# Kernel tuning notes

Measured on AMD Instinct MI355X. Metric: run time of the kernel, lower is better.

The kernel has to match this reference:

```python
import jax, jax.numpy as jnp
import numpy as np

B, T, E, H = 4, 2048, 1024, 16
S = E // H

def setup_inputs() -> dict:
    key = jax.random.key(0)
    ks = jax.random.split(key, 4)
    x = jax.random.normal(ks[0], (B, T, E), dtype=jnp.float32)
    Wk = jax.random.normal(ks[1], (E, E), dtype=jnp.float32) * (E ** -0.5)
    Wq = jax.random.normal(ks[2], (E, E), dtype=jnp.float32) * (E ** -0.5)
    Wo = jax.random.normal(ks[3], (E, E), dtype=jnp.float32) * (E ** -0.5)
    bo = jnp.zeros((E,), dtype=jnp.float32)
    return {"x": x, "Wk": Wk, "Wq": Wq, "Wo": Wo, "bo": bo}

def reference(x, Wk, Wq, Wo, bo):
    b, t, e = x.shape
    h, s = H, E // H
    scale = e ** (-0.25)  # original scales q and k each by e**(1/4)
    k = (x @ Wk).reshape(b, t, h, s).transpose(0, 2, 1, 3)  # bhts
    q = (x @ Wq).reshape(b, t, h, s).transpose(0, 2, 1, 3)
    # FAITHFUL to source: values use the KEYS projection (bug in original)
    v = (x @ Wk).reshape(b, t, h, s).transpose(0, 2, 1, 3)
    dot = jnp.einsum('bhqd,bhkd->bhqk', q * scale, k * scale)
    attn = jax.nn.softmax(dot, axis=-1)
    out = jnp.einsum('bhqk,bhkd->bhqd', attn, v)
    out = out.transpose(0, 2, 1, 3).reshape(b, t, e)
    return out @ Wo + bo
```

## Files before the change

kernel.cpp:

```cpp
#include <hip/hip_runtime.h>
#include <hip/hip_bf16.h>
#include <stdint.h>

static constexpr int kB = 4;
static constexpr int kT = 2048;
static constexpr int kE = 1024;
static constexpr int kH = 16;
static constexpr int kS = 64;
static constexpr int kRows = kB * kT;

typedef __attribute__((ext_vector_type(4)))  float    f32x4;
typedef __attribute__((ext_vector_type(16))) float    f32x16;
typedef __attribute__((ext_vector_type(4)))  float    float4v;
typedef __attribute__((ext_vector_type(8)))  __bf16   bf16x8;
typedef __attribute__((ext_vector_type(8)))  short    short8v;
typedef __attribute__((ext_vector_type(4)))  short    short4v;
typedef __attribute__((ext_vector_type(2)))  unsigned u32x2;

typedef const __attribute__((address_space(1))) void gvoid_t;
typedef __attribute__((address_space(3))) void lvoid_t;

__device__ __forceinline__ short f2bf(float f) {
  union { float f; unsigned u; } c; c.f = f;
  unsigned r = (c.u + 0x7FFFu + ((c.u >> 16) & 1u)) >> 16;
  return (short)(r & 0xFFFFu);
}

__device__ __forceinline__ short bfc(float f) {
  union { __bf16 b; short s; } u; u.b = (__bf16)f; return u.s;
}

__device__ __forceinline__ unsigned cvt_pk(float lo, float hi) {
  unsigned r;
  asm("v_cvt_pk_bf16_f32 %0, %1, %2" : "=v"(r) : "v"(lo), "v"(hi));
  return r;
}

__device__ __forceinline__ void plane_swap(unsigned& a, unsigned& b) {
  asm("v_permlane32_swap_b32 %0, %1" : "+v"(a), "+v"(b));
}

#if __has_builtin(__builtin_amdgcn_exp2f)
__device__ __forceinline__ float fexp2(float x) { return __builtin_amdgcn_exp2f(x); }
#else
__device__ __forceinline__ float fexp2(float x) { return exp2f(x); }
#endif

__global__ void cvt_bf16(const float* __restrict__ in, short* __restrict__ out) {
  size_t i = (size_t)(blockIdx.x * blockDim.x + threadIdx.x) * 4;
  float4v x = *(const float4v*)(in + i);
  short4v o;
  o[0] = f2bf(x[0]); o[1] = f2bf(x[1]); o[2] = f2bf(x[2]); o[3] = f2bf(x[3]);
  *(short4v*)(out + i) = o;
}

__global__ void transpose_cvt(const float* __restrict__ W, short* __restrict__ WT) {
  __shared__ float tile[32][33];
  const int tx = threadIdx.x & 31, ty = threadIdx.x >> 5;
  const int c = blockIdx.x * 32, r = blockIdx.y * 32;
  #pragma unroll
  for (int i = ty; i < 32; i += 8)
    tile[i][tx] = W[(size_t)(r + i) * kE + c + tx];
  __syncthreads();
  #pragma unroll
  for (int i = ty; i < 32; i += 8)
    WT[(size_t)(c + i) * kE + r + tx] = f2bf(tile[tx][i]);
}

__global__ __launch_bounds__(256)
void transv(const short* __restrict__ Kb, short* __restrict__ KT) {
  __shared__ short tile[64][72];
  const int tid = threadIdx.x;
  const int bh = blockIdx.y;
  const int t0 = blockIdx.x * 64;
  const size_t base = (size_t)(bh >> 4) * kT * kE + (size_t)(bh & 15) * kS;
  #pragma unroll
  for (int i = 0; i < 2; ++i) {
    const int row = i * 32 + (tid >> 3), c = (tid & 7) * 8;
    *(short8v*)&tile[row][c] =
        *(const short8v*)(Kb + base + (size_t)(t0 + row) * kE + c);
  }
  __syncthreads();
  #pragma unroll
  for (int i = 0; i < 2; ++i) {
    const int s = i * 32 + (tid >> 3), c = (tid & 7) * 8;
    short8v o;
    #pragma unroll
    for (int j = 0; j < 8; ++j) o[j] = tile[c + j][s];
    *(short8v*)(KT + ((size_t)bh * 64 + s) * kT + t0 + c) = o;
  }
}

__global__ __launch_bounds__(256)
void gemm_kq(const short* __restrict__ A, const short* __restrict__ BT,
             short* __restrict__ Kb, short* __restrict__ Qb, float qs) {
  __shared__ short As[128 * 64];
  __shared__ short Bs[128 * 64];
  const int tid = threadIdx.x;
  const int w = tid >> 6, lane = tid & 63;
  const int g = lane >> 4, lr = lane & 15;
  const int bid = blockIdx.x;
  const int id = (bid & 7) * 128 + (bid >> 3);
  const int n0 = (id & 15) * 128, m0 = (id >> 4) * 128;
  const int wr = w >> 1, wc = w & 1;
  const int srow = lane >> 3, sch = lane & 7;
  const int swz = lr & 7;

  f32x4 acc[4][4];
  #pragma unroll
  for (int m = 0; m < 4; ++m)
    #pragma unroll
    for (int n = 0; n < 4; ++n)
      #pragma unroll
      for (int r = 0; r < 4; ++r) acc[m][n][r] = 0.f;

  for (int kt = 0; kt < kE; kt += 64) {
    #pragma unroll
    for (int i = 0; i < 4; ++i) {
      const int slot = w * 4 + i;
      const int row = slot * 8 + srow;
      const int sc = sch ^ srow;
      __builtin_amdgcn_global_load_lds(
          (gvoid_t*)(A + (size_t)(m0 + row) * kE + kt + 8 * sc),
          (lvoid_t*)(As + slot * 512), 16, 0, 0);
      __builtin_amdgcn_global_load_lds(
          (gvoid_t*)(BT + (size_t)(n0 + row) * kE + kt + 8 * sc),
          (lvoid_t*)(Bs + slot * 512), 16, 0, 0);
    }
    __syncthreads();
    #pragma unroll
    for (int kk = 0; kk < 2; ++kk) {
      bf16x8 af[4], bfr[4];
      #pragma unroll
      for (int m = 0; m < 4; ++m)
        af[m] = *(const bf16x8*)(As + (wr * 64 + m * 16 + lr) * 64 + (((4 * kk + g) ^ swz) << 3));
      #pragma unroll
      for (int n = 0; n < 4; ++n)
        bfr[n] = *(const bf16x8*)(Bs + (wc * 64 + n * 16 + lr) * 64 + (((4 * kk + g) ^ swz) << 3));
      __builtin_amdgcn_s_setprio(1);
      #pragma unroll
      for (int m = 0; m < 4; ++m)
        #pragma unroll
        for (int n = 0; n < 4; ++n)
          acc[m][n] = __builtin_amdgcn_mfma_f32_16x16x32_bf16(af[m], bfr[n], acc[m][n], 0, 0, 0);
      __builtin_amdgcn_s_setprio(0);
    }
    __syncthreads();
  }

  short* C = (n0 < 1024) ? Kb : Qb;
  const float scale = (n0 < 1024) ? 1.0f : qs;
  const int crow = m0 + wr * 64, ccol = (n0 & 1023) + wc * 64;
  #pragma unroll
  for (int m = 0; m < 4; ++m)
    #pragma unroll
    for (int n = 0; n < 4; ++n)
      #pragma unroll
      for (int r = 0; r < 4; ++r)
        C[(size_t)(crow + m * 16 + 4 * g + r) * kE + ccol + n * 16 + lr] =
            bfc(acc[m][n][r] * scale);
}

__global__ __launch_bounds__(256)
void gemm_bt(const short* __restrict__ A, const short* __restrict__ BT,
             float* __restrict__ C, const float* __restrict__ bias,
             int M, int N, int K) {
  __shared__ short As[128 * 64];
  __shared__ short Bs[128 * 64];
  const int tid = threadIdx.x;
  const int w = tid >> 6, lane = tid & 63;
  const int g = lane >> 4, lr = lane & 15;
  const int bid = blockIdx.x;
  const int id = (bid & 7) * 64 + (bid >> 3);
  const int n0 = (id & 7) * 128, m0 = (id >> 3) * 128;
  const int wr = w >> 1, wc = w & 1;
  const int srow = lane >> 3, sch = lane & 7;
  const int swz = lr & 7;

  f32x4 acc[4][4];
  #pragma unroll
  for (int m = 0; m < 4; ++m)
    #pragma unroll
    for (int n = 0; n < 4; ++n)
      #pragma unroll
      for (int r = 0; r < 4; ++r) acc[m][n][r] = 0.f;

  for (int kt = 0; kt < K; kt += 64) {
    #pragma unroll
    for (int i = 0; i < 4; ++i) {
      const int slot = w * 4 + i;
      const int row = slot * 8 + srow;
      const int sc = sch ^ srow;
      __builtin_amdgcn_global_load_lds(
          (gvoid_t*)(A + (size_t)(m0 + row) * K + kt + 8 * sc),
          (lvoid_t*)(As + slot * 512), 16, 0, 0);
      __builtin_amdgcn_global_load_lds(
          (gvoid_t*)(BT + (size_t)(n0 + row) * K + kt + 8 * sc),
          (lvoid_t*)(Bs + slot * 512), 16, 0, 0);
    }
    __syncthreads();
    #pragma unroll
    for (int kk = 0; kk < 2; ++kk) {
      bf16x8 af[4], bfr[4];
      #pragma unroll
      for (int m = 0; m < 4; ++m)
        af[m] = *(const bf16x8*)(As + (wr * 64 + m * 16 + lr) * 64 + (((4 * kk + g) ^ swz) << 3));
      #pragma unroll
      for (int n = 0; n < 4; ++n)
        bfr[n] = *(const bf16x8*)(Bs + (wc * 64 + n * 16 + lr) * 64 + (((4 * kk + g) ^ swz) << 3));
      __builtin_amdgcn_s_setprio(1);
      #pragma unroll
      for (int m = 0; m < 4; ++m)
        #pragma unroll
        for (int n = 0; n < 4; ++n)
          acc[m][n] = __builtin_amdgcn_mfma_f32_16x16x32_bf16(af[m], bfr[n], acc[m][n], 0, 0, 0);
      __builtin_amdgcn_s_setprio(0);
    }
    __syncthreads();
  }

  const int crow = m0 + wr * 64, ccol = n0 + wc * 64;
  float bv[4];
  #pragma unroll
  for (int n = 0; n < 4; ++n) bv[n] = bias[ccol + n * 16 + lr];
  #pragma unroll
  for (int m = 0; m < 4; ++m)
    #pragma unroll
    for (int n = 0; n < 4; ++n)
      #pragma unroll
      for (int r = 0; r < 4; ++r)
        C[(size_t)(crow + m * 16 + 4 * g + r) * N + ccol + n * 16 + lr] =
            acc[m][n][r] + bv[n];
}

__global__ __launch_bounds__(256, 4)
void attn_kernel(const short* Qb, const short* __restrict__ Kb,
                 const short* __restrict__ KT, short* AO) {
  __shared__ short SM[16384];

  const int tid = threadIdx.x;
  const int w = tid >> 6, lane = tid & 63;
  const int l31 = lane & 31, hi = lane >> 5;
  const int swz = l31 & 7;
  const int bid = blockIdx.x;
  const int id = (bid & 7) * 128 + (bid >> 3);
  const int q0 = (id & 15) * 128;
  const int bh = id >> 4;
  const size_t base = (size_t)(bh >> 4) * kT * kE + (size_t)(bh & 15) * kS;
  const short* Kbh = Kb + base;
  const short* KTbh = KT + (size_t)bh * 64 * kT;

  const int srow_lo = lane >> 3, sch = lane & 7;

  #pragma unroll
  for (int i = 0; i < 2; ++i) {
    const int slot = w * 2 + i, row = slot * 8 + srow_lo;
    const int sc = sch ^ (row & 7);
    __builtin_amdgcn_global_load_lds(
        (gvoid_t*)(Kbh + (size_t)row * kE + 8 * sc),
        (lvoid_t*)(SM + slot * 512), 16, 0, 0);
    __builtin_amdgcn_global_load_lds(
        (gvoid_t*)(KTbh + (size_t)row * kT + 8 * sc),
        (lvoid_t*)(SM + 8192 + slot * 512), 16, 0, 0);
  }

  bf16x8 qB[4];
  #pragma unroll
  for (int ks = 0; ks < 4; ++ks)
    qB[ks] = *(const bf16x8*)(Qb + base +
        (size_t)(q0 + w * 32 + l31) * kE + ks * 16 + hi * 8);

  f32x16 oacc[2];
  #pragma unroll
  for (int r = 0; r < 16; ++r) { oacc[0][r] = 0.f; oacc[1][r] = 0.f; }
  float lsum = 0.f;

  for (int t = 0; t < 32; ++t) {
    __syncthreads();

    if (t < 31) {
      const short* kbt = Kbh + (size_t)(t + 1) * 64 * kE;
      const short* vtt = KTbh + (size_t)(t + 1) * 64;
      short* KtN = SM + ((t + 1) & 1) * 4096;
      short* VtN = SM + 8192 + ((t + 1) & 1) * 4096;
      #pragma unroll
      for (int i = 0; i < 2; ++i) {
        const int slot = w * 2 + i, row = slot * 8 + srow_lo;
        const int sc = sch ^ (row & 7);
        __builtin_amdgcn_global_load_lds(
            (gvoid_t*)(kbt + (size_t)row * kE + 8 * sc),
            (lvoid_t*)(KtN + slot * 512), 16, 0, 0);
        __builtin_amdgcn_global_load_lds(
            (gvoid_t*)(vtt + (size_t)row * kT + 8 * sc),
            (lvoid_t*)(VtN + slot * 512), 16, 0, 0);
      }
    }

    const short* KtC = SM + (t & 1) * 4096;
    const short* VtC = SM + 8192 + (t & 1) * 4096;

    f32x16 sacc[2];
    #pragma unroll
    for (int r = 0; r < 16; ++r) { sacc[0][r] = 0.f; sacc[1][r] = 0.f; }
    #pragma unroll
    for (int ks = 0; ks < 4; ++ks) {
      const int pc = ((2 * ks + hi) ^ swz) << 3;
      bf16x8 kf0 = *(const bf16x8*)(KtC + (l31)      * 64 + pc);
      bf16x8 kf1 = *(const bf16x8*)(KtC + (32 + l31) * 64 + pc);
      __builtin_amdgcn_s_setprio(1);
      sacc[0] = __builtin_amdgcn_mfma_f32_32x32x16_bf16(kf0, qB[ks], sacc[0], 0, 0, 0);
      sacc[1] = __builtin_amdgcn_mfma_f32_32x32x16_bf16(kf1, qB[ks], sacc[1], 0, 0, 0);
      __builtin_amdgcn_s_setprio(0);
    }

    union { unsigned u[4]; bf16x8 v; } pf[4];
    #pragma unroll
    for (int kvf = 0; kvf < 2; ++kvf) {
      float pe[16];
      #pragma unroll
      for (int r = 0; r < 16; ++r) {
        pe[r] = fexp2(sacc[kvf][r]);
        lsum += pe[r];
      }
      #pragma unroll
      for (int sub = 0; sub < 2; ++sub) {
        unsigned a0 = cvt_pk(pe[8 * sub + 0], pe[8 * sub + 1]);
        unsigned b0 = cvt_pk(pe[8 * sub + 4], pe[8 * sub + 5]);
        plane_swap(a0, b0);
        unsigned a1 = cvt_pk(pe[8 * sub + 2], pe[8 * sub + 3]);
        unsigned b1 = cvt_pk(pe[8 * sub + 6], pe[8 * sub + 7]);
        plane_swap(a1, b1);
        pf[2 * kvf + sub].u[0] = a0;
        pf[2 * kvf + sub].u[1] = a1;
        pf[2 * kvf + sub].u[2] = b0;
        pf[2 * kvf + sub].u[3] = b1;
      }
    }

    #pragma unroll
    for (int ks = 0; ks < 4; ++ks) {
      const int pc = ((2 * ks + hi) ^ swz) << 3;
      bf16x8 vf0 = *(const bf16x8*)(VtC + (l31)      * 64 + pc);
      bf16x8 vf1 = *(const bf16x8*)(VtC + (32 + l31) * 64 + pc);
      __builtin_amdgcn_s_setprio(1);
      oacc[0] = __builtin_amdgcn_mfma_f32_32x32x16_bf16(vf0, pf[ks].v, oacc[0], 0, 0, 0);
      oacc[1] = __builtin_amdgcn_mfma_f32_32x32x16_bf16(vf1, pf[ks].v, oacc[1], 0, 0, 0);
      __builtin_amdgcn_s_setprio(0);
    }
  }

  __syncthreads();

  const float ltot = lsum + __shfl_xor(lsum, 32);
  const float inv = 1.f / ltot;
  short* OtW = SM + w * 2176;
  #pragma unroll
  for (int sf = 0; sf < 2; ++sf)
    #pragma unroll
    for (int c = 0; c < 4; ++c) {
      u32x2 e;
      e[0] = cvt_pk(oacc[sf][4 * c + 0] * inv, oacc[sf][4 * c + 1] * inv);
      e[1] = cvt_pk(oacc[sf][4 * c + 2] * inv, oacc[sf][4 * c + 3] * inv);
      *(u32x2*)(OtW + l31 * 68 + sf * 32 + 8 * c + 4 * hi) = e;
    }
  __builtin_amdgcn_s_barrier();
  #pragma unroll
  for (int i = 0; i < 8; ++i) {
    const int row = i * 4 + (lane >> 4);
    u32x2 v = *(const u32x2*)(OtW + row * 68 + (lane & 15) * 4);
    *(u32x2*)(AO + base + (size_t)(q0 + w * 32 + row) * kE + (lane & 15) * 4) = v;
  }
}

extern "C" void kernel_launch(void* const* d_in, const int* in_sizes, int n_in,
                              void* d_out, int out_size, void* d_ws, size_t ws_size,
                              hipStream_t stream) {
  const float* x  = (const float*)d_in[0];
  const float* Wk = (const float*)d_in[1];
  const float* Wq = (const float*)d_in[2];
  const float* Wo = (const float*)d_in[3];
  const float* bo = (const float*)d_in[4];
  float* out = (float*)d_out;

  const size_t nXE = (size_t)kRows * kE;
  const size_t nW  = (size_t)kE * kE;

  short* Xb   = (short*)d_ws;
  short* Kb   = Xb   + nXE;
  short* Qb   = Kb   + nXE;
  short* WkqT = Qb   + nXE;
  short* WoT  = WkqT + 2 * nW;
  short* KTb  = Xb;
  short* AO   = Qb;

  cvt_bf16<<<dim3(nXE / (4 * 256)), 256, 0, stream>>>(x, Xb);
  transpose_cvt<<<dim3(32, 32), 256, 0, stream>>>(Wk, WkqT);
  transpose_cvt<<<dim3(32, 32), 256, 0, stream>>>(Wq, WkqT + nW);
  transpose_cvt<<<dim3(32, 32), 256, 0, stream>>>(Wo, WoT);

  gemm_kq<<<dim3(1024), 256, 0, stream>>>(
      Xb, WkqT, Kb, Qb, 0.03125f * 1.44269504f);

  transv<<<dim3(kT / 64, kB * kH), 256, 0, stream>>>(Kb, KTb);

  attn_kernel<<<dim3(1024), 256, 0, stream>>>(Qb, Kb, KTb, AO);

  gemm_bt<<<dim3(512), 256, 0, stream>>>(
      AO, WoT, out, bo, kRows, kE, kE);
}
```

Before: 177.4 us.

## Fuse prep conversions into one kernel and emit transposed K from GEMM epilogue

```diff
diff --git a/kernel.cpp b/kernel.cpp
--- a/kernel.cpp
+++ b/kernel.cpp
@@ -16,6 +16,7 @@
 typedef __attribute__((ext_vector_type(8)))  short    short8v;
 typedef __attribute__((ext_vector_type(4)))  short    short4v;
 typedef __attribute__((ext_vector_type(2)))  unsigned u32x2;
+typedef __attribute__((ext_vector_type(4)))  unsigned u32x4;
 
 typedef const __attribute__((address_space(1))) void gvoid_t;
 typedef __attribute__((address_space(3))) void lvoid_t;
@@ -46,18 +47,27 @@
 __device__ __forceinline__ float fexp2(float x) { return exp2f(x); }
 #endif
 
-__global__ void cvt_bf16(const float* __restrict__ in, short* __restrict__ out) {
-  size_t i = (size_t)(blockIdx.x * blockDim.x + threadIdx.x) * 4;
-  float4v x = *(const float4v*)(in + i);
-  short4v o;
-  o[0] = f2bf(x[0]); o[1] = f2bf(x[1]); o[2] = f2bf(x[2]); o[3] = f2bf(x[3]);
-  *(short4v*)(out + i) = o;
-}
-
-__global__ void transpose_cvt(const float* __restrict__ W, short* __restrict__ WT) {
+__global__ __launch_bounds__(256)
+void prep(const float* __restrict__ x, const float* __restrict__ Wk,
+          const float* __restrict__ Wq, const float* __restrict__ Wo,
+          short* __restrict__ Xb, short* __restrict__ WkqT,
+          short* __restrict__ WoT) {
+  const int bid = blockIdx.x;
+  if (bid < 8192) {
+    size_t i = ((size_t)bid * 256 + threadIdx.x) * 4;
+    float4v v = *(const float4v*)(x + i);
+    short4v o;
+    o[0] = f2bf(v[0]); o[1] = f2bf(v[1]); o[2] = f2bf(v[2]); o[3] = f2bf(v[3]);
+    *(short4v*)(Xb + i) = o;
+    return;
+  }
   __shared__ float tile[32][33];
+  const int tb = bid - 8192;
+  const int which = tb >> 10, t = tb & 1023;
+  const float* W = (which == 0) ? Wk : ((which == 1) ? Wq : Wo);
+  short* WT = (which == 0) ? WkqT : ((which == 1) ? (WkqT + kE * kE) : WoT);
   const int tx = threadIdx.x & 31, ty = threadIdx.x >> 5;
-  const int c = blockIdx.x * 32, r = blockIdx.y * 32;
+  const int c = (t & 31) * 32, r = (t >> 5) * 32;
   #pragma unroll
   for (int i = ty; i < 32; i += 8)
     tile[i][tx] = W[(size_t)(r + i) * kE + c + tx];
@@ -68,34 +78,12 @@
 }
 
 __global__ __launch_bounds__(256)
-void transv(const short* __restrict__ Kb, short* __restrict__ KT) {
-  __shared__ short tile[64][72];
-  const int tid = threadIdx.x;
-  const int bh = blockIdx.y;
-  const int t0 = blockIdx.x * 64;
-  const size_t base = (size_t)(bh >> 4) * kT * kE + (size_t)(bh & 15) * kS;
-  #pragma unroll
-  for (int i = 0; i < 2; ++i) {
-    const int row = i * 32 + (tid >> 3), c = (tid & 7) * 8;
-    *(short8v*)&tile[row][c] =
-        *(const short8v*)(Kb + base + (size_t)(t0 + row) * kE + c);
-  }
-  __syncthreads();
-  #pragma unroll
-  for (int i = 0; i < 2; ++i) {
-    const int s = i * 32 + (tid >> 3), c = (tid & 7) * 8;
-    short8v o;
-    #pragma unroll
-    for (int j = 0; j < 8; ++j) o[j] = tile[c + j][s];
-    *(short8v*)(KT + ((size_t)bh * 64 + s) * kT + t0 + c) = o;
-  }
-}
-
-__global__ __launch_bounds__(256)
 void gemm_kq(const short* __restrict__ A, const short* __restrict__ BT,
-             short* __restrict__ Kb, short* __restrict__ Qb, float qs) {
-  __shared__ short As[128 * 64];
-  __shared__ short Bs[128 * 64];
+             short* __restrict__ Kb, short* __restrict__ Qb,
+             short* __restrict__ KT, float qs) {
+  __shared__ short SMp[16384];
+  short* As = SMp;
+  short* Bs = SMp + 8192;
   const int tid = threadIdx.x;
   const int w = tid >> 6, lane = tid & 63;
   const int g = lane >> 4, lr = lane & 15;
@@ -159,6 +147,37 @@
       for (int r = 0; r < 4; ++r)
         C[(size_t)(crow + m * 16 + 4 * g + r) * kE + ccol + n * 16 + lr] =
             bfc(acc[m][n][r] * scale);
+
+  if (n0 < 1024) {
+    const int b = m0 >> 11;
+    const int tloc = m0 & 2047;
+    short* Lt = SMp;
+    #pragma unroll
+    for (int half = 0; half < 2; ++half) {
+      __syncthreads();
+      if (wc == half) {
+        #pragma unroll
+        for (int m = 0; m < 4; ++m)
+          #pragma unroll
+          for (int n = 0; n < 4; ++n) {
+            u32x2 e;
+            e[0] = cvt_pk(acc[m][n][0], acc[m][n][1]);
+            e[1] = cvt_pk(acc[m][n][2], acc[m][n][3]);
+            *(u32x2*)(Lt + (n * 16 + lr) * 136 + wr * 64 + m * 16 + 4 * g) = e;
+          }
+      }
+      __syncthreads();
+      const int sc = tid >> 2;
+      const int h = (n0 >> 6) + half;
+      short* ktrow = KT + ((size_t)(b * 16 + h) * 64 + sc) * kT + tloc;
+      #pragma unroll
+      for (int i = 0; i < 4; ++i) {
+        const int t4 = (tid & 3) * 32 + i * 8;
+        u32x4 v = *(const u32x4*)(Lt + sc * 136 + t4);
+        *(u32x4*)(ktrow + t4) = v;
+      }
+    }
+  }
 }
 
 __global__ __launch_bounds__(256)
@@ -390,18 +409,14 @@
   short* Qb   = Kb   + nXE;
   short* WkqT = Qb   + nXE;
   short* WoT  = WkqT + 2 * nW;
-  short* KTb  = Xb;
+  short* KTb  = (short*)d_out;
   short* AO   = Qb;
 
-  cvt_bf16<<<dim3(nXE / (4 * 256)), 256, 0, stream>>>(x, Xb);
-  transpose_cvt<<<dim3(32, 32), 256, 0, stream>>>(Wk, WkqT);
-  transpose_cvt<<<dim3(32, 32), 256, 0, stream>>>(Wq, WkqT + nW);
-  transpose_cvt<<<dim3(32, 32), 256, 0, stream>>>(Wo, WoT);
+  prep<<<dim3(8192 + 3 * 1024), 256, 0, stream>>>(
+      x, Wk, Wq, Wo, Xb, WkqT, WoT);
 
   gemm_kq<<<dim3(1024), 256, 0, stream>>>(
-      Xb, WkqT, Kb, Qb, 0.03125f * 1.44269504f);
-
-  transv<<<dim3(kT / 64, kB * kH), 256, 0, stream>>>(Kb, KTb);
+      Xb, WkqT, Kb, Qb, KTb, 0.03125f * 1.44269504f);
 
   attn_kernel<<<dim3(1024), 256, 0, stream>>>(Qb, Kb, KTb, AO);
 
```

Result: faster. 172.5 us (-2.8%).
